# Kernel tuning notes

Measured on AMD Instinct MI355X. Metric: run time of the kernel, lower is better.

The kernel has to match this reference:

```python
import jax, jax.numpy as jnp
import numpy as np

B, T, M, Q = 1024, 336, 1, 9
DFF, H, L = 7, 1024, 2
D_IN = DFF + M      # decoder input per step
D_OUT = M * Q       # quantile outputs per step


def setup_inputs() -> dict:
    key = jax.random.key(0)
    ks = jax.random.split(key, 16)
    s = 1.0 / np.sqrt(H)

    def rn(k, shape, scale):
        return (jax.random.normal(k, shape, jnp.float32) * scale).astype(jnp.float32)

    return {
        "batchsize": B,
        "Y_teacher": rn(ks[0], (B, T, M), 1.0),
        "inp_y": rn(ks[1], (B, 1, M), 1.0),
        "h": rn(ks[2], (L, B, H), 0.1),
        "c": rn(ks[3], (L, B, H), 0.1),
        "future_features": rn(ks[4], (B, T, DFF), 1.0),
        "horizon_span": T,
        "teacher_forcing": 0,
        "teacher_forcing_prob": 0,
        # LSTM layer 0 (input size D_IN) and layer 1 (input size H), PyTorch i,f,g,o gate order
        "W_ih0": rn(ks[5], (4 * H, D_IN), s),
        "W_hh0": rn(ks[6], (4 * H, H), s),
        "b_ih0": rn(ks[7], (4 * H,), s),
        "b_hh0": rn(ks[8], (4 * H,), s),
        "W_ih1": rn(ks[9], (4 * H, H), s),
        "W_hh1": rn(ks[10], (4 * H, H), s),
        "b_ih1": rn(ks[11], (4 * H,), s),
        "b_hh1": rn(ks[12], (4 * H,), s),
        # output projection d_hidden -> M*Q
        "W_out": rn(ks[13], (D_OUT, H), s),
        "b_out": rn(ks[14], (D_OUT,), s),
    }


def reference(batchsize, Y_teacher, inp_y, h, c, future_features, horizon_span,
              teacher_forcing, teacher_forcing_prob,
              W_ih0, W_hh0, b_ih0, b_hh0, W_ih1, W_hh1, b_ih1, b_hh1,
              W_out, b_out):
    m = inp_y.shape[-1]
    Wih = (W_ih0, W_ih1)
    Whh = (W_hh0, W_hh1)
    bih = (b_ih0, b_ih1)
    bhh = (b_hh0, b_hh1)

    def step(carry, f_t):
        hs, cs, y_prev = carry            # hs,cs: [L,B,H]; y_prev: [B,M]; f_t: [B,DFF]
        x = jnp.concatenate([y_prev, f_t], axis=-1)   # [B, D_IN]
        new_h, new_c = [], []
        for l in range(len(Wih)):
            gates = x @ Wih[l].T + bih[l] + hs[l] @ Whh[l].T + bhh[l]  # [B, 4H]
            i_, f_, g_, o_ = jnp.split(gates, 4, axis=-1)
            c_new = jax.nn.sigmoid(f_) * cs[l] + jax.nn.sigmoid(i_) * jnp.tanh(g_)
            h_new = jax.nn.sigmoid(o_) * jnp.tanh(c_new)
            new_h.append(h_new)
            new_c.append(c_new)
            x = h_new
        y = x @ W_out.T + b_out           # [B, M*Q]
        return (jnp.stack(new_h), jnp.stack(new_c), y[:, :m]), y

    ff = jnp.swapaxes(future_features, 0, 1)          # [T, B, DFF]
    _, ys = jax.lax.scan(step, (h, c, inp_y[:, 0, :]), ff)
    out = jnp.swapaxes(ys, 0, 1)                      # [B, T, M*Q]
    return out.reshape(batchsize, horizon_span, m, -1)
```

## Files before the change

kernel.cpp:

```cpp
#include <hip/hip_runtime.h>

typedef _Float16 f16;
typedef __attribute__((ext_vector_type(8))) _Float16 f16x8;
typedef __attribute__((ext_vector_type(4))) float f32x4;

#define NBATCH 1024
#define NH 1024
#define NT 336
#define NDFF 7
#define NQ 9
#define K0 1088
#define K1 2048
#define OUTSTRIDE (NT * NQ)

__device__ __forceinline__ float sigf(float x) { return 1.0f / (1.0f + __expf(-x)); }
__device__ __forceinline__ float tanhfast(float x) { return 1.0f - 2.0f / (__expf(2.0f * x) + 1.0f); }

__device__ __forceinline__ void gll16(const void* g, void* l) {
  __builtin_amdgcn_global_load_lds((const __attribute__((address_space(1))) void*)g,
                                   (__attribute__((address_space(3))) void*)l, 16, 0, 0);
}

__global__ void pack_w0(const float* __restrict__ Wih0, const float* __restrict__ Whh0,
                        f16* __restrict__ Wp0) {
  const int idx = blockIdx.x * 256 + threadIdx.x;
  const int pr = idx / K0;
  const int dk = idx - pr * K0;
  const int cb = pr >> 7, p = pr & 127;
  const int gate = (p >> 4) & 3;
  const int hl = ((p >> 6) << 4) | (p & 15);
  const int j = (gate << 10) + (cb << 5) + hl;
  const int sk = (dk & ~63) | ((dk & 63) ^ ((p & 7) << 3));
  float v;
  if (sk < 8) v = Wih0[j * 8 + sk];
  else if (sk < 64) v = 0.0f;
  else v = Whh0[(size_t)j * NH + (sk - 64)];
  Wp0[idx] = (f16)v;
}

__global__ void pack_w1(const float* __restrict__ Wih1, const float* __restrict__ Whh1,
                        f16* __restrict__ Wp1) {
  const int idx = blockIdx.x * 256 + threadIdx.x;
  const int pr = idx >> 11;
  const int dk = idx & 2047;
  const int cb = pr >> 7, p = pr & 127;
  const int gate = (p >> 4) & 3;
  const int hl = ((p >> 6) << 4) | (p & 15);
  const int j = (gate << 10) + (cb << 5) + hl;
  const int sk = (dk & ~63) | ((dk & 63) ^ ((p & 7) << 3));
  const float v = (sk < 1024) ? Wih1[(size_t)j * NH + sk]
                              : Whh1[(size_t)j * NH + (sk - 1024)];
  Wp1[idx] = (f16)v;
}

__global__ void pack_bias(const float* __restrict__ a0, const float* __restrict__ b0,
                          const float* __restrict__ a1, const float* __restrict__ b1,
                          float* __restrict__ bias0, float* __restrict__ bias1) {
  const int j = blockIdx.x * 256 + threadIdx.x;
  if (j < 4096) { bias0[j] = a0[j] + b0[j]; bias1[j] = a1[j] + b1[j]; }
}

__global__ void init_state(const float* __restrict__ h_in, const float* __restrict__ c_in,
                           f16* __restrict__ h0, f16* __restrict__ h1,
                           float* __restrict__ c0, float* __restrict__ c1) {
  const int idx = blockIdx.x * 256 + threadIdx.x;
  const int l = idx >> 20;
  const int rc = idx & 1048575;
  const int row = rc >> 10;
  const int dk = idx & 1023;
  const int sk = (dk & ~63) | ((dk & 63) ^ ((row & 7) << 3));
  const float hv = h_in[((size_t)l << 20) + ((size_t)row << 10) + sk];
  if (l == 0) { h0[rc] = (f16)hv; c0[rc] = c_in[idx]; }
  else        { h1[rc] = (f16)hv; c1[rc] = c_in[idx]; }
}

__global__ void final_y(const float* __restrict__ ypartT, const float* __restrict__ bout,
                        float* __restrict__ dout) {
  const int idx = blockIdx.x * 256 + threadIdx.x;
  const int row = idx & 1023;
  const int q = idx >> 10;
  float s = bout[q];
#pragma unroll
  for (int nb2 = 0; nb2 < 32; ++nb2) s += ypartT[(((q << 5) + nb2) << 10) + row];
  dout[(size_t)row * OUTSTRIDE + 335 * NQ + q] = s;
}

template <int IS_S1>
__global__ __launch_bounds__(256, 1) void step_kernel(
    const f16* __restrict__ Wp, const float* __restrict__ bias,
    const f16* __restrict__ hA, const f16* __restrict__ hA2,
    float* __restrict__ cbuf, f16* __restrict__ hout,
    const float* __restrict__ ff, const float* __restrict__ inpy,
    float* __restrict__ ypartT, const float* __restrict__ Wout,
    const float* __restrict__ bout, float* __restrict__ dout, int t) {
  constexpr int KDIM = IS_S1 ? K1 : K0;
  constexpr int NKT = KDIM / 64;
  constexpr int LDSZ = IS_S1 ? (98304 + 128 * 33 * 4) : 98304;
  __shared__ __align__(16) unsigned char lds8[LDSZ];

  const int tid = threadIdx.x;
  const int wv = tid >> 6;
  const int ln = tid & 63;
  const int wr = wv >> 1, wc = wv & 1;
  const int blk = blockIdx.x;
  const int rb = (blk >> 3) & 7;
  const int cb = (blk & 7) * 4 + (blk >> 6);
  const int row0 = rb * 128;
  const int hcol0 = cb * 32;

  auto stageB = [&](int kt, int buf) {
#pragma unroll
    for (int i = 0; i < 4; ++i) {
      const int ci = wv * 4 + i;
      const int tr = ci * 8 + (ln >> 3);
      const f16* g = Wp + (size_t)(cb * 128 + tr) * KDIM + kt * 64 + (ln & 7) * 8;
      gll16(g, lds8 + buf * 32768 + 16384 + ci * 1024);
    }
  };
  auto stageA = [&](int kt, int buf) {
    const f16* src;
    int kb;
    if (IS_S1) {
      if (kt < 16) { src = hA; kb = kt * 64; }
      else { src = hA2; kb = (kt - 16) * 64; }
    } else { src = hA; kb = (kt - 1) * 64; }
#pragma unroll
    for (int i = 0; i < 4; ++i) {
      const int ci = wv * 4 + i;
      const int r = ci * 8 + (ln >> 3);
      const f16* g = src + (size_t)(row0 + r) * NH + kb + (ln & 7) * 8;
      gll16(g, lds8 + buf * 32768 + ci * 1024);
    }
  };

  if (!IS_S1) {
    if (tid < 128) {
      const int row = row0 + tid;
      float y0;
      if (t == 0) {
        y0 = inpy[row];
      } else {
        y0 = bout[0];
        const float* yp = ypartT + row;
#pragma unroll
        for (int nb2 = 0; nb2 < 32; ++nb2) y0 += yp[nb2 << 10];
      }
      const float* fsrc = ff + ((size_t)row * NT + t) * NDFF;
      f16x8 xv;
      xv[0] = (f16)y0;
#pragma unroll
      for (int jj = 0; jj < 7; ++jj) xv[1 + jj] = (f16)fsrc[jj];
      *(f16x8*)(lds8 + tid * 128 + ((tid & 7) << 4)) = xv;
    }
    f16x8 zv;
#pragma unroll
    for (int jj = 0; jj < 8; ++jj) zv[jj] = (f16)0.0f;
    for (int idx = tid; idx < 128 * 7; idx += 256) {
      const int r = idx / 7;
      const int ch = 1 + (idx - r * 7);
      *(f16x8*)(lds8 + r * 128 + ((ch ^ (r & 7)) << 4)) = zv;
    }
    if (t > 0 && cb < NQ && tid < 128) {
      const int q = cb;
      const int row = row0 + tid;
      float s = bout[q];
      const float* yp = ypartT + ((size_t)(q << 5) << 10) + row;
#pragma unroll
      for (int nb2 = 0; nb2 < 32; ++nb2) s += yp[nb2 << 10];
      dout[(size_t)row * OUTSTRIDE + (t - 1) * NQ + q] = s;
    }
    stageB(0, 0);
    stageA(1, 1); stageB(1, 1);
  } else {
    stageA(0, 0); stageB(0, 0);
    stageA(1, 1); stageB(1, 1);
  }
  asm volatile("s_waitcnt lgkmcnt(0)" ::: "memory");

  f32x4 acc[4][4];
  const f32x4 zf = {0.0f, 0.0f, 0.0f, 0.0f};
#pragma unroll
  for (int m = 0; m < 4; ++m)
#pragma unroll
    for (int n = 0; n < 4; ++n) acc[m][n] = zf;

  const int lanerow = ln & 15;
  const int xm = (ln & 7) << 4;
  const int kgrp = (ln >> 4) << 4;
  int bc = 0;

  for (int kt = 0; kt < NKT; ++kt) {
    __builtin_amdgcn_sched_barrier(0);
    if (kt + 1 < NKT) {
      asm volatile("s_waitcnt vmcnt(8)" ::: "memory");
    } else {
      asm volatile("s_waitcnt vmcnt(0)" ::: "memory");
    }
    __builtin_amdgcn_s_barrier();
    __builtin_amdgcn_sched_barrier(0);
    if (kt + 2 < NKT) {
      const int nb = (bc == 0) ? 2 : bc - 1;
      stageA(kt + 2, nb);
      stageB(kt + 2, nb);
    }
    const unsigned char* Ab = lds8 + bc * 32768;
    const unsigned char* Bb = Ab + 16384;
#pragma unroll
    for (int ks = 0; ks < 2; ++ks) {
      const int kb = (kgrp + ks * 64) ^ xm;
      f16x8 afr[4], bfr[4];
#pragma unroll
      for (int m = 0; m < 4; ++m)
        afr[m] = *(const f16x8*)(Ab + (wr * 64 + m * 16 + lanerow) * 128 + kb);
#pragma unroll
      for (int n = 0; n < 4; ++n)
        bfr[n] = *(const f16x8*)(Bb + (wc * 64 + n * 16 + lanerow) * 128 + kb);
      __builtin_amdgcn_s_setprio(1);
#pragma unroll
      for (int m = 0; m < 4; ++m)
#pragma unroll
        for (int n = 0; n < 4; ++n)
          acc[m][n] = __builtin_amdgcn_mfma_f32_16x16x32_f16(afr[m], bfr[n], acc[m][n], 0, 0, 0);
      __builtin_amdgcn_s_setprio(0);
    }
    bc = (bc == 2) ? 0 : bc + 1;
  }

  float* hbuf = (float*)(lds8 + 98304);
  const int hcol = hcol0 + wc * 16 + lanerow;
  const float bi = bias[hcol];
  const float bff = bias[NH + hcol];
  const float bg = bias[2 * NH + hcol];
  const float bo = bias[3 * NH + hcol];
#pragma unroll
  for (int m = 0; m < 4; ++m) {
    const f32x4 vi = acc[m][0];
    const f32x4 vf = acc[m][1];
    const f32x4 vg = acc[m][2];
    const f32x4 vo = acc[m][3];
#pragma unroll
    for (int r = 0; r < 4; ++r) {
      const int rloc = wr * 64 + m * 16 + ((ln >> 4) << 2) + r;
      const int row = row0 + rloc;
      const size_t cidx = (size_t)row * NH + hcol;
      const float c_old = cbuf[cidx];
      const float ig = sigf(vi[r] + bi);
      const float fg = sigf(vf[r] + bff);
      const float gg = tanhfast(vg[r] + bg);
      const float og = sigf(vo[r] + bo);
      const float cn = fg * c_old + ig * gg;
      const float hn = og * tanhfast(cn);
      cbuf[cidx] = cn;
      *(f16*)((unsigned char*)hout + (size_t)row * 2048 + ((hcol >> 6) << 7) +
              (((hcol & 63) << 1) ^ ((row & 7) << 4))) = (f16)hn;
      if (IS_S1) hbuf[rloc * 33 + wc * 16 + lanerow] = hn;
    }
  }
  if (IS_S1) {
    __syncthreads();
    for (int task = tid; task < 128 * NQ; task += 256) {
      const int rloc = task & 127;
      const int q = task >> 7;
      const float* wq = Wout + q * NH + hcol0;
      float s = 0.0f;
#pragma unroll
      for (int c2 = 0; c2 < 32; ++c2) s += hbuf[rloc * 33 + c2] * wq[c2];
      ypartT[(size_t)((q << 5) + cb) * 1024 + row0 + rloc] = s;
    }
  }
}

extern "C" void kernel_launch(void* const* d_in, const int* in_sizes, int n_in,
                              void* d_out, int out_size, void* d_ws, size_t ws_size,
                              hipStream_t stream) {
  const float* inpy = (const float*)d_in[2];
  const float* h_in = (const float*)d_in[3];
  const float* c_in = (const float*)d_in[4];
  const float* ff   = (const float*)d_in[5];
  const float* Wih0 = (const float*)d_in[9];
  const float* Whh0 = (const float*)d_in[10];
  const float* bih0 = (const float*)d_in[11];
  const float* bhh0 = (const float*)d_in[12];
  const float* Wih1 = (const float*)d_in[13];
  const float* Whh1 = (const float*)d_in[14];
  const float* bih1 = (const float*)d_in[15];
  const float* bhh1 = (const float*)d_in[16];
  const float* Wout = (const float*)d_in[17];
  const float* bout = (const float*)d_in[18];
  float* dout = (float*)d_out;

  unsigned char* ws = (unsigned char*)d_ws;
  size_t off = 0;
  auto alloc = [&](size_t bytes) -> void* {
    void* p = ws + off;
    off += (bytes + 255) & ~(size_t)255;
    return p;
  };
  f16* Wp0 = (f16*)alloc((size_t)4096 * K0 * 2);
  f16* Wp1 = (f16*)alloc((size_t)4096 * K1 * 2);
  f16* h0b0 = (f16*)alloc((size_t)NBATCH * NH * 2);
  f16* h0b1 = (f16*)alloc((size_t)NBATCH * NH * 2);
  f16* h1b0 = (f16*)alloc((size_t)NBATCH * NH * 2);
  f16* h1b1 = (f16*)alloc((size_t)NBATCH * NH * 2);
  float* c0 = (float*)alloc((size_t)NBATCH * NH * 4);
  float* c1 = (float*)alloc((size_t)NBATCH * NH * 4);
  float* bias0 = (float*)alloc(4096 * 4);
  float* bias1 = (float*)alloc(4096 * 4);
  float* ypartT = (float*)alloc((size_t)NQ * 32 * 1024 * 4);
  f16* h0b[2] = {h0b0, h0b1};
  f16* h1b[2] = {h1b0, h1b1};

  pack_w0<<<(4096 * K0) / 256, 256, 0, stream>>>(Wih0, Whh0, Wp0);
  pack_w1<<<(4096 * K1) / 256, 256, 0, stream>>>(Wih1, Whh1, Wp1);
  pack_bias<<<16, 256, 0, stream>>>(bih0, bhh0, bih1, bhh1, bias0, bias1);
  init_state<<<(2 * NBATCH * NH) / 256, 256, 0, stream>>>(h_in, c_in, h0b[0], h1b[0], c0, c1);

  for (int t = 0; t < NT; ++t) {
    const int p = t & 1;
    step_kernel<0><<<256, 256, 0, stream>>>(Wp0, bias0, h0b[p], nullptr, c0, h0b[1 - p],
                                            ff, inpy, ypartT, nullptr, bout, dout, t);
    step_kernel<1><<<256, 256, 0, stream>>>(Wp1, bias1, h0b[1 - p], h1b[p], c1, h1b[1 - p],
                                            nullptr, nullptr, ypartT, Wout, bout, dout, t);
  }
  final_y<<<36, 256, 0, stream>>>(ypartT, bout, dout);
}
```

Measured before the change: 15.05 ms.

## Replace per-step kernel launches with one persistent kernel using per-row-block counters

Fuses the 672 per-timestep launches into a single persistent kernel of 256 blocks. Blocks synchronise through per-row-block atomic counters with spin-waits, and the cell states stay in registers for all steps. Loads of the next layer's weights and of the h tiles are software-pipelined across layer boundaries, so the global barriers overlap with useful work. In exchange it depends on all 256 blocks being co-resident and on correct cross-block memory visibility (h loads use cache-bypass bits), which risks deadlock or stale reads.

```diff
diff --git a/kernel.cpp b/kernel.cpp
--- a/kernel.cpp
+++ b/kernel.cpp
@@ -16,9 +16,19 @@
 __device__ __forceinline__ float sigf(float x) { return 1.0f / (1.0f + __expf(-x)); }
 __device__ __forceinline__ float tanhfast(float x) { return 1.0f - 2.0f / (__expf(2.0f * x) + 1.0f); }
 
-__device__ __forceinline__ void gll16(const void* g, void* l) {
+__device__ __forceinline__ void gll_w(const void* g, void* l) {
   __builtin_amdgcn_global_load_lds((const __attribute__((address_space(1))) void*)g,
                                    (__attribute__((address_space(3))) void*)l, 16, 0, 0);
+}
+__device__ __forceinline__ void gll_c(const void* g, void* l) {
+  __builtin_amdgcn_global_load_lds((const __attribute__((address_space(1))) void*)g,
+                                   (__attribute__((address_space(3))) void*)l, 16, 0, 17);
+}
+
+__device__ __forceinline__ void spinGE(unsigned int* c, unsigned int tgt) {
+  while (__hip_atomic_load(c, __ATOMIC_RELAXED, __HIP_MEMORY_SCOPE_AGENT) < tgt) {
+    __builtin_amdgcn_s_sleep(2);
+  }
 }
 
 __global__ void pack_w0(const float* __restrict__ Wih0, const float* __restrict__ Whh0,
@@ -53,16 +63,17 @@
   Wp1[idx] = (f16)v;
 }
 
-__global__ void pack_bias(const float* __restrict__ a0, const float* __restrict__ b0,
+__global__ void pack_misc(const float* __restrict__ a0, const float* __restrict__ b0,
                           const float* __restrict__ a1, const float* __restrict__ b1,
-                          float* __restrict__ bias0, float* __restrict__ bias1) {
+                          float* __restrict__ bias0, float* __restrict__ bias1,
+                          unsigned int* __restrict__ cnt) {
   const int j = blockIdx.x * 256 + threadIdx.x;
   if (j < 4096) { bias0[j] = a0[j] + b0[j]; bias1[j] = a1[j] + b1[j]; }
-}
-
-__global__ void init_state(const float* __restrict__ h_in, const float* __restrict__ c_in,
-                           f16* __restrict__ h0, f16* __restrict__ h1,
-                           float* __restrict__ c0, float* __restrict__ c1) {
+  if (j < 16) cnt[j] = 0;
+}
+
+__global__ void init_h(const float* __restrict__ h_in,
+                       f16* __restrict__ h0, f16* __restrict__ h1) {
   const int idx = blockIdx.x * 256 + threadIdx.x;
   const int l = idx >> 20;
   const int rc = idx & 1048575;
@@ -70,8 +81,8 @@
   const int dk = idx & 1023;
   const int sk = (dk & ~63) | ((dk & 63) ^ ((row & 7) << 3));
   const float hv = h_in[((size_t)l << 20) + ((size_t)row << 10) + sk];
-  if (l == 0) { h0[rc] = (f16)hv; c0[rc] = c_in[idx]; }
-  else        { h1[rc] = (f16)hv; c1[rc] = c_in[idx]; }
+  if (l == 0) h0[rc] = (f16)hv;
+  else        h1[rc] = (f16)hv;
 }
 
 __global__ void final_y(const float* __restrict__ ypartT, const float* __restrict__ bout,
@@ -85,18 +96,18 @@
   dout[(size_t)row * OUTSTRIDE + 335 * NQ + q] = s;
 }
 
-template <int IS_S1>
-__global__ __launch_bounds__(256, 1) void step_kernel(
-    const f16* __restrict__ Wp, const float* __restrict__ bias,
-    const f16* __restrict__ hA, const f16* __restrict__ hA2,
-    float* __restrict__ cbuf, f16* __restrict__ hout,
+__global__ __launch_bounds__(256, 1) void persist(
+    const f16* __restrict__ Wp0, const f16* __restrict__ Wp1,
+    const float* __restrict__ bias0, const float* __restrict__ bias1,
+    f16* __restrict__ h0b0, f16* __restrict__ h0b1,
+    f16* __restrict__ h1b0, f16* __restrict__ h1b1,
+    unsigned int* __restrict__ cnt,
     const float* __restrict__ ff, const float* __restrict__ inpy,
     float* __restrict__ ypartT, const float* __restrict__ Wout,
-    const float* __restrict__ bout, float* __restrict__ dout, int t) {
-  constexpr int KDIM = IS_S1 ? K1 : K0;
-  constexpr int NKT = KDIM / 64;
-  constexpr int LDSZ = IS_S1 ? (98304 + 128 * 33 * 4) : 98304;
-  __shared__ __align__(16) unsigned char lds8[LDSZ];
+    const float* __restrict__ bout, const float* __restrict__ c_in,
+    float* __restrict__ dout) {
+  __shared__ __align__(16) unsigned char lds8[98304 + 128 * 33 * 4];
+  float* hbuf = (float*)(lds8 + 98304);
 
   const int tid = threadIdx.x;
   const int wv = tid >> 6;
@@ -107,75 +118,50 @@
   const int cb = (blk & 7) * 4 + (blk >> 6);
   const int row0 = rb * 128;
   const int hcol0 = cb * 32;
-
-  auto stageB = [&](int kt, int buf) {
+  unsigned int* aCnt = cnt + rb;
+  unsigned int* bCnt = cnt + 8 + rb;
+
+  f16* h0arr[2] = {h0b0, h0b1};
+  f16* h1arr[2] = {h1b0, h1b1};
+
+  const int lanerow = ln & 15;
+  const int xm = (ln & 7) << 4;
+  const int kgrp = (ln >> 4) << 4;
+  const int hcol = hcol0 + wc * 16 + lanerow;
+
+  float c0r[4][4], c1r[4][4];
+#pragma unroll
+  for (int m = 0; m < 4; ++m)
+#pragma unroll
+    for (int r = 0; r < 4; ++r) {
+      const int row = row0 + wr * 64 + m * 16 + ((ln >> 4) << 2) + r;
+      c0r[m][r] = c_in[(size_t)row * NH + hcol];
+      c1r[m][r] = c_in[(size_t)(NBATCH * NH) + (size_t)row * NH + hcol];
+    }
+
+  const float b0i = bias0[hcol], b0f = bias0[NH + hcol],
+              b0g = bias0[2 * NH + hcol], b0o = bias0[3 * NH + hcol];
+  const float b1i = bias1[hcol], b1f = bias1[NH + hcol],
+              b1g = bias1[2 * NH + hcol], b1o = bias1[3 * NH + hcol];
+
+  auto stW = [&](const f16* W, int KDIM, int kt, int buf) {
 #pragma unroll
     for (int i = 0; i < 4; ++i) {
       const int ci = wv * 4 + i;
       const int tr = ci * 8 + (ln >> 3);
-      const f16* g = Wp + (size_t)(cb * 128 + tr) * KDIM + kt * 64 + (ln & 7) * 8;
-      gll16(g, lds8 + buf * 32768 + 16384 + ci * 1024);
+      gll_w(W + (size_t)(cb * 128 + tr) * KDIM + kt * 64 + (ln & 7) * 8,
+            lds8 + buf * 32768 + 16384 + ci * 1024);
     }
   };
-  auto stageA = [&](int kt, int buf) {
-    const f16* src;
-    int kb;
-    if (IS_S1) {
-      if (kt < 16) { src = hA; kb = kt * 64; }
-      else { src = hA2; kb = (kt - 16) * 64; }
-    } else { src = hA; kb = (kt - 1) * 64; }
+  auto stH = [&](const f16* h, int kb, int buf) {
 #pragma unroll
     for (int i = 0; i < 4; ++i) {
       const int ci = wv * 4 + i;
       const int r = ci * 8 + (ln >> 3);
-      const f16* g = src + (size_t)(row0 + r) * NH + kb + (ln & 7) * 8;
-      gll16(g, lds8 + buf * 32768 + ci * 1024);
+      gll_c(h + (((size_t)(row0 + r)) << 10) + kb + (ln & 7) * 8,
+            lds8 + buf * 32768 + ci * 1024);
     }
   };
-
-  if (!IS_S1) {
-    if (tid < 128) {
-      const int row = row0 + tid;
-      float y0;
-      if (t == 0) {
-        y0 = inpy[row];
-      } else {
-        y0 = bout[0];
-        const float* yp = ypartT + row;
-#pragma unroll
-        for (int nb2 = 0; nb2 < 32; ++nb2) y0 += yp[nb2 << 10];
-      }
-      const float* fsrc = ff + ((size_t)row * NT + t) * NDFF;
-      f16x8 xv;
-      xv[0] = (f16)y0;
-#pragma unroll
-      for (int jj = 0; jj < 7; ++jj) xv[1 + jj] = (f16)fsrc[jj];
-      *(f16x8*)(lds8 + tid * 128 + ((tid & 7) << 4)) = xv;
-    }
-    f16x8 zv;
-#pragma unroll
-    for (int jj = 0; jj < 8; ++jj) zv[jj] = (f16)0.0f;
-    for (int idx = tid; idx < 128 * 7; idx += 256) {
-      const int r = idx / 7;
-      const int ch = 1 + (idx - r * 7);
-      *(f16x8*)(lds8 + r * 128 + ((ch ^ (r & 7)) << 4)) = zv;
-    }
-    if (t > 0 && cb < NQ && tid < 128) {
-      const int q = cb;
-      const int row = row0 + tid;
-      float s = bout[q];
-      const float* yp = ypartT + ((size_t)(q << 5) << 10) + row;
-#pragma unroll
-      for (int nb2 = 0; nb2 < 32; ++nb2) s += yp[nb2 << 10];
-      dout[(size_t)row * OUTSTRIDE + (t - 1) * NQ + q] = s;
-    }
-    stageB(0, 0);
-    stageA(1, 1); stageB(1, 1);
-  } else {
-    stageA(0, 0); stageB(0, 0);
-    stageA(1, 1); stageB(1, 1);
-  }
-  asm volatile("s_waitcnt lgkmcnt(0)" ::: "memory");
 
   f32x4 acc[4][4];
   const f32x4 zf = {0.0f, 0.0f, 0.0f, 0.0f};
@@ -184,26 +170,8 @@
 #pragma unroll
     for (int n = 0; n < 4; ++n) acc[m][n] = zf;
 
-  const int lanerow = ln & 15;
-  const int xm = (ln & 7) << 4;
-  const int kgrp = (ln >> 4) << 4;
-  int bc = 0;
-
-  for (int kt = 0; kt < NKT; ++kt) {
-    __builtin_amdgcn_sched_barrier(0);
-    if (kt + 1 < NKT) {
-      asm volatile("s_waitcnt vmcnt(8)" ::: "memory");
-    } else {
-      asm volatile("s_waitcnt vmcnt(0)" ::: "memory");
-    }
-    __builtin_amdgcn_s_barrier();
-    __builtin_amdgcn_sched_barrier(0);
-    if (kt + 2 < NKT) {
-      const int nb = (bc == 0) ? 2 : bc - 1;
-      stageA(kt + 2, nb);
-      stageB(kt + 2, nb);
-    }
-    const unsigned char* Ab = lds8 + bc * 32768;
+  auto compute = [&](int bufc) {
+    const unsigned char* Ab = lds8 + bufc * 32768;
     const unsigned char* Bb = Ab + 16384;
 #pragma unroll
     for (int ks = 0; ks < 2; ++ks) {
@@ -223,40 +191,153 @@
           acc[m][n] = __builtin_amdgcn_mfma_f32_16x16x32_f16(afr[m], bfr[n], acc[m][n], 0, 0, 0);
       __builtin_amdgcn_s_setprio(0);
     }
-    bc = (bc == 2) ? 0 : bc + 1;
-  }
-
-  float* hbuf = (float*)(lds8 + 98304);
-  const int hcol = hcol0 + wc * 16 + lanerow;
-  const float bi = bias[hcol];
-  const float bff = bias[NH + hcol];
-  const float bg = bias[2 * NH + hcol];
-  const float bo = bias[3 * NH + hcol];
-#pragma unroll
-  for (int m = 0; m < 4; ++m) {
-    const f32x4 vi = acc[m][0];
-    const f32x4 vf = acc[m][1];
-    const f32x4 vg = acc[m][2];
-    const f32x4 vo = acc[m][3];
-#pragma unroll
-    for (int r = 0; r < 4; ++r) {
-      const int rloc = wr * 64 + m * 16 + ((ln >> 4) << 2) + r;
-      const int row = row0 + rloc;
-      const size_t cidx = (size_t)row * NH + hcol;
-      const float c_old = cbuf[cidx];
-      const float ig = sigf(vi[r] + bi);
-      const float fg = sigf(vf[r] + bff);
-      const float gg = tanhfast(vg[r] + bg);
-      const float og = sigf(vo[r] + bo);
-      const float cn = fg * c_old + ig * gg;
-      const float hn = og * tanhfast(cn);
-      cbuf[cidx] = cn;
-      *(f16*)((unsigned char*)hout + (size_t)row * 2048 + ((hcol >> 6) << 7) +
-              (((hcol & 63) << 1) ^ ((row & 7) << 4))) = (f16)hn;
-      if (IS_S1) hbuf[rloc * 33 + wc * 16 + lanerow] = hn;
-    }
-  }
-  if (IS_S1) {
+  };
+
+  stH(h0arr[0], 0, 0);  stW(Wp0, K0, 1, 0);
+  stH(h0arr[0], 64, 1); stW(Wp0, K0, 2, 1);
+
+  int sb = 0;
+
+  for (int t = 0; t < NT; ++t) {
+    const int p = t & 1;
+    const f16* h0prev = h0arr[p];
+    f16* h0new = h0arr[1 - p];
+    const f16* h1prev = h1arr[p];
+    f16* h1new = h1arr[1 - p];
+
+    for (int it = 0; it < 17; ++it) {
+      __builtin_amdgcn_sched_barrier(0);
+      if (it == 15) asm volatile("s_waitcnt vmcnt(4) lgkmcnt(0)" ::: "memory");
+      else          asm volatile("s_waitcnt vmcnt(8) lgkmcnt(0)" ::: "memory");
+      __builtin_amdgcn_s_barrier();
+      __builtin_amdgcn_sched_barrier(0);
+      const int bufc = sb;
+      const int bufs = (sb + 2 >= 3) ? sb - 1 : sb + 2;
+
+      if (it == 14) {
+        if (t > 0) {
+          if (tid == 0) spinGE(bCnt, 32u * (unsigned)t);
+          __builtin_amdgcn_s_barrier();
+          __builtin_amdgcn_sched_barrier(0);
+        }
+        unsigned char* xb = lds8 + bufs * 32768;
+        if (tid < 128) {
+          const int row = row0 + tid;
+          float y0;
+          if (t == 0) {
+            y0 = inpy[row];
+          } else {
+            y0 = bout[0];
+#pragma unroll
+            for (int nb2 = 0; nb2 < 32; ++nb2)
+              y0 += __hip_atomic_load(ypartT + (nb2 << 10) + row,
+                                      __ATOMIC_RELAXED, __HIP_MEMORY_SCOPE_AGENT);
+          }
+          const float* fsrc = ff + ((size_t)row * NT + t) * NDFF;
+          f16x8 xv;
+          xv[0] = (f16)y0;
+#pragma unroll
+          for (int jj = 0; jj < 7; ++jj) xv[1 + jj] = (f16)fsrc[jj];
+          *(f16x8*)(xb + tid * 128 + ((tid & 7) << 4)) = xv;
+        }
+        f16x8 zv;
+#pragma unroll
+        for (int jj = 0; jj < 8; ++jj) zv[jj] = (f16)0.0f;
+        for (int idx = tid; idx < 128 * 7; idx += 256) {
+          const int r = idx / 7;
+          const int ch = 1 + (idx - r * 7);
+          *(f16x8*)(xb + r * 128 + ((ch ^ (r & 7)) << 4)) = zv;
+        }
+        if (t > 0 && cb < NQ && tid < 128) {
+          const int row = row0 + tid;
+          float s = bout[cb];
+#pragma unroll
+          for (int nb2 = 0; nb2 < 32; ++nb2)
+            s += __hip_atomic_load(ypartT + (((cb << 5) + nb2) << 10) + row,
+                                   __ATOMIC_RELAXED, __HIP_MEMORY_SCOPE_AGENT);
+          dout[(size_t)row * OUTSTRIDE + (t - 1) * NQ + cb] = s;
+        }
+        stW(Wp0, K0, 0, bufs);
+      } else {
+        const int s = it + 2;
+        if (s <= 15)      { stH(h0prev, s * 64, bufs); stW(Wp0, K0, s + 1, bufs); }
+        else if (s == 17) { stH(h1prev, 0, bufs);      stW(Wp1, K1, 16, bufs); }
+        else              { stH(h1prev, 64, bufs);     stW(Wp1, K1, 17, bufs); }
+      }
+      compute(bufc);
+      sb = (bufc + 1 >= 3) ? 0 : bufc + 1;
+    }
+
+#pragma unroll
+    for (int m = 0; m < 4; ++m) {
+      const f32x4 vi = acc[m][0], vf = acc[m][1], vg = acc[m][2], vo = acc[m][3];
+#pragma unroll
+      for (int r = 0; r < 4; ++r) {
+        const int rloc = wr * 64 + m * 16 + ((ln >> 4) << 2) + r;
+        const int row = row0 + rloc;
+        const float ig = sigf(vi[r] + b0i);
+        const float fg = sigf(vf[r] + b0f);
+        const float gg = tanhfast(vg[r] + b0g);
+        const float og = sigf(vo[r] + b0o);
+        const float cn = fg * c0r[m][r] + ig * gg;
+        c0r[m][r] = cn;
+        const f16 hn = (f16)(og * tanhfast(cn));
+        unsigned short hb = __builtin_bit_cast(unsigned short, hn);
+        unsigned short* dst = (unsigned short*)((unsigned char*)h0new + (size_t)row * 2048 +
+                              ((hcol >> 6) << 7) + (((hcol & 63) << 1) ^ ((row & 7) << 4)));
+        __hip_atomic_store(dst, hb, __ATOMIC_RELAXED, __HIP_MEMORY_SCOPE_AGENT);
+      }
+      acc[m][0] = zf; acc[m][1] = zf; acc[m][2] = zf; acc[m][3] = zf;
+    }
+    asm volatile("s_waitcnt vmcnt(0)" ::: "memory");
+    __syncthreads();
+    if (tid == 0)
+      __hip_atomic_fetch_add(aCnt, 1u, __ATOMIC_RELAXED, __HIP_MEMORY_SCOPE_AGENT);
+
+    for (int it = 0; it < 32; ++it) {
+      __builtin_amdgcn_sched_barrier(0);
+      asm volatile("s_waitcnt vmcnt(8) lgkmcnt(0)" ::: "memory");
+      __builtin_amdgcn_s_barrier();
+      __builtin_amdgcn_sched_barrier(0);
+      const int bufc = sb;
+      const int bufs = (sb + 2 >= 3) ? sb - 1 : sb + 2;
+
+      if (it == 14) {
+        if (tid == 0) spinGE(aCnt, 32u * (unsigned)(t + 1));
+        __builtin_amdgcn_s_barrier();
+        __builtin_amdgcn_sched_barrier(0);
+      }
+      const int s = it + 2;
+      if (s <= 15)      { stH(h1prev, s * 64, bufs);       stW(Wp1, K1, 16 + s, bufs); }
+      else if (s <= 31) { stH(h0new, (s - 16) * 64, bufs); stW(Wp1, K1, s - 16, bufs); }
+      else              { stH(h0new, (s - 32) * 64, bufs); stW(Wp0, K0, s - 31, bufs); }
+      compute(bufc);
+      sb = (bufc + 1 >= 3) ? 0 : bufc + 1;
+    }
+
+#pragma unroll
+    for (int m = 0; m < 4; ++m) {
+      const f32x4 vi = acc[m][0], vf = acc[m][1], vg = acc[m][2], vo = acc[m][3];
+#pragma unroll
+      for (int r = 0; r < 4; ++r) {
+        const int rloc = wr * 64 + m * 16 + ((ln >> 4) << 2) + r;
+        const int row = row0 + rloc;
+        const float ig = sigf(vi[r] + b1i);
+        const float fg = sigf(vf[r] + b1f);
+        const float gg = tanhfast(vg[r] + b1g);
+        const float og = sigf(vo[r] + b1o);
+        const float cn = fg * c1r[m][r] + ig * gg;
+        c1r[m][r] = cn;
+        const float hnf = og * tanhfast(cn);
+        const f16 hn = (f16)hnf;
+        unsigned short hb = __builtin_bit_cast(unsigned short, hn);
+        unsigned short* dst = (unsigned short*)((unsigned char*)h1new + (size_t)row * 2048 +
+                              ((hcol >> 6) << 7) + (((hcol & 63) << 1) ^ ((row & 7) << 4)));
+        __hip_atomic_store(dst, hb, __ATOMIC_RELAXED, __HIP_MEMORY_SCOPE_AGENT);
+        hbuf[rloc * 33 + wc * 16 + lanerow] = hnf;
+      }
+      acc[m][0] = zf; acc[m][1] = zf; acc[m][2] = zf; acc[m][3] = zf;
+    }
     __syncthreads();
     for (int task = tid; task < 128 * NQ; task += 256) {
       const int rloc = task & 127;
@@ -265,8 +346,13 @@
       float s = 0.0f;
 #pragma unroll
       for (int c2 = 0; c2 < 32; ++c2) s += hbuf[rloc * 33 + c2] * wq[c2];
-      ypartT[(size_t)((q << 5) + cb) * 1024 + row0 + rloc] = s;
-    }
+      __hip_atomic_store(ypartT + (size_t)((q << 5) + cb) * 1024 + row0 + rloc, s,
+                         __ATOMIC_RELAXED, __HIP_MEMORY_SCOPE_AGENT);
+    }
+    asm volatile("s_waitcnt vmcnt(0)" ::: "memory");
+    __syncthreads();
+    if (tid == 0)
+      __hip_atomic_fetch_add(bCnt, 1u, __ATOMIC_RELAXED, __HIP_MEMORY_SCOPE_AGENT);
   }
 }
 
@@ -302,25 +388,18 @@
   f16* h0b1 = (f16*)alloc((size_t)NBATCH * NH * 2);
   f16* h1b0 = (f16*)alloc((size_t)NBATCH * NH * 2);
   f16* h1b1 = (f16*)alloc((size_t)NBATCH * NH * 2);
-  float* c0 = (float*)alloc((size_t)NBATCH * NH * 4);
-  float* c1 = (float*)alloc((size_t)NBATCH * NH * 4);
   float* bias0 = (float*)alloc(4096 * 4);
   float* bias1 = (float*)alloc(4096 * 4);
   float* ypartT = (float*)alloc((size_t)NQ * 32 * 1024 * 4);
-  f16* h0b[2] = {h0b0, h0b1};
-  f16* h1b[2] = {h1b0, h1b1};
+  unsigned int* cnt = (unsigned int*)alloc(64);
 
   pack_w0<<<(4096 * K0) / 256, 256, 0, stream>>>(Wih0, Whh0, Wp0);
   pack_w1<<<(4096 * K1) / 256, 256, 0, stream>>>(Wih1, Whh1, Wp1);
-  pack_bias<<<16, 256, 0, stream>>>(bih0, bhh0, bih1, bhh1, bias0, bias1);
-  init_state<<<(2 * NBATCH * NH) / 256, 256, 0, stream>>>(h_in, c_in, h0b[0], h1b[0], c0, c1);
-
-  for (int t = 0; t < NT; ++t) {
-    const int p = t & 1;
-    step_kernel<0><<<256, 256, 0, stream>>>(Wp0, bias0, h0b[p], nullptr, c0, h0b[1 - p],
-                                            ff, inpy, ypartT, nullptr, bout, dout, t);
-    step_kernel<1><<<256, 256, 0, stream>>>(Wp1, bias1, h0b[1 - p], h1b[p], c1, h1b[1 - p],
-                                            nullptr, nullptr, ypartT, Wout, bout, dout, t);
-  }
+  pack_misc<<<16, 256, 0, stream>>>(bih0, bhh0, bih1, bhh1, bias0, bias1, cnt);
+  init_h<<<(2 * NBATCH * NH) / 256, 256, 0, stream>>>(h_in, h0b0, h1b0);
+
+  persist<<<256, 256, 0, stream>>>(Wp0, Wp1, bias0, bias1, h0b0, h0b1, h1b0, h1b1,
+                                   cnt, ff, inpy, ypartT, Wout, bout, c_in, dout);
+
   final_y<<<36, 256, 0, stream>>>(ypartT, bout, dout);
 }
```

Result: slower. 18.93 ms (+25.7%).

## Use 128-wide K tiles, lane-packed cell state and LDS-staged vector h stores

Applied to the files above, without the earlier changes.

Each K stage now covers 128 elements and uses two buffers instead of three 64-wide buffers, waiting for all loads and barriering once per stage. Layer 0's 8-wide input chunk gets its own LDS area and is computed first. The fp32 cell state is repacked at init so each lane reads and writes contiguous addresses, replacing scattered row-major accesses. New h values are staged through LDS and written as 16-byte f16 vectors instead of single scattered f16 stores. The aim is fewer barriers and more coalesced state traffic, but a full vmcnt(0) wait every stage may hide less load latency.

```diff
diff --git a/kernel.cpp b/kernel.cpp
--- a/kernel.cpp
+++ b/kernel.cpp
@@ -12,11 +12,12 @@
 #define K0 1088
 #define K1 2048
 #define OUTSTRIDE (NT * NQ)
+#define XAOFF 131072
 
 __device__ __forceinline__ float sigf(float x) { return 1.0f / (1.0f + __expf(-x)); }
 __device__ __forceinline__ float tanhfast(float x) { return 1.0f - 2.0f / (__expf(2.0f * x) + 1.0f); }
 
-__device__ __forceinline__ void gll16(const void* g, void* l) {
+__device__ __forceinline__ void gll(const void* g, void* l) {
   __builtin_amdgcn_global_load_lds((const __attribute__((address_space(1))) void*)g,
                                    (__attribute__((address_space(3))) void*)l, 16, 0, 0);
 }
@@ -60,9 +61,8 @@
   if (j < 4096) { bias0[j] = a0[j] + b0[j]; bias1[j] = a1[j] + b1[j]; }
 }
 
-__global__ void init_state(const float* __restrict__ h_in, const float* __restrict__ c_in,
-                           f16* __restrict__ h0, f16* __restrict__ h1,
-                           float* __restrict__ c0, float* __restrict__ c1) {
+__global__ void init_h(const float* __restrict__ h_in,
+                       f16* __restrict__ h0, f16* __restrict__ h1) {
   const int idx = blockIdx.x * 256 + threadIdx.x;
   const int l = idx >> 20;
   const int rc = idx & 1048575;
@@ -70,8 +70,24 @@
   const int dk = idx & 1023;
   const int sk = (dk & ~63) | ((dk & 63) ^ ((row & 7) << 3));
   const float hv = h_in[((size_t)l << 20) + ((size_t)row << 10) + sk];
-  if (l == 0) { h0[rc] = (f16)hv; c0[rc] = c_in[idx]; }
-  else        { h1[rc] = (f16)hv; c1[rc] = c_in[idx]; }
+  if (l == 0) h0[rc] = (f16)hv;
+  else        h1[rc] = (f16)hv;
+}
+
+__global__ void init_c(const float* __restrict__ c_in, float* __restrict__ c0p,
+                       float* __restrict__ c1p) {
+  const int idx = blockIdx.x * 256 + threadIdx.x;
+  const int l = idx >> 20;
+  const int rem = idx & 1048575;
+  const int ln = rem & 63;
+  const int j = (rem >> 6) & 15;
+  const int wv = (rem >> 10) & 3;
+  const int cb = (rem >> 12) & 31;
+  const int rb = rem >> 17;
+  const int row = rb * 128 + (wv >> 1) * 64 + (j >> 2) * 16 + ((ln >> 4) & 3) * 4 + (j & 3);
+  const int col = cb * 32 + (wv & 1) * 16 + (ln & 15);
+  const float v = c_in[((size_t)l << 20) + ((size_t)row << 10) + col];
+  if (l == 0) c0p[rem] = v; else c1p[rem] = v;
 }
 
 __global__ void final_y(const float* __restrict__ ypartT, const float* __restrict__ bout,
@@ -85,18 +101,17 @@
   dout[(size_t)row * OUTSTRIDE + 335 * NQ + q] = s;
 }
 
-template <int IS_S1>
+template <int L>
 __global__ __launch_bounds__(256, 1) void step_kernel(
     const f16* __restrict__ Wp, const float* __restrict__ bias,
-    const f16* __restrict__ hA, const f16* __restrict__ hA2,
-    float* __restrict__ cbuf, f16* __restrict__ hout,
+    const f16* __restrict__ hA0, const f16* __restrict__ hA1,
+    f16* __restrict__ hout, float* __restrict__ cpk,
     const float* __restrict__ ff, const float* __restrict__ inpy,
     float* __restrict__ ypartT, const float* __restrict__ Wout,
     const float* __restrict__ bout, float* __restrict__ dout, int t) {
-  constexpr int KDIM = IS_S1 ? K1 : K0;
-  constexpr int NKT = KDIM / 64;
-  constexpr int LDSZ = IS_S1 ? (98304 + 128 * 33 * 4) : 98304;
-  __shared__ __align__(16) unsigned char lds8[LDSZ];
+  constexpr int KDIM = L ? K1 : K0;
+  constexpr int NTILE = L ? 16 : 9;
+  __shared__ __align__(16) unsigned char lds8[147456];
 
   const int tid = threadIdx.x;
   const int wv = tid >> 6;
@@ -108,32 +123,66 @@
   const int row0 = rb * 128;
   const int hcol0 = cb * 32;
 
-  auto stageB = [&](int kt, int buf) {
-#pragma unroll
-    for (int i = 0; i < 4; ++i) {
-      const int ci = wv * 4 + i;
-      const int tr = ci * 8 + (ln >> 3);
-      const f16* g = Wp + (size_t)(cb * 128 + tr) * KDIM + kt * 64 + (ln & 7) * 8;
-      gll16(g, lds8 + buf * 32768 + 16384 + ci * 1024);
+  const int lanerow = ln & 15;
+  const int xm = (ln & 7) << 4;
+  const int kgrp = (ln >> 4) << 4;
+  const int hcol = hcol0 + wc * 16 + lanerow;
+
+  auto stage128 = [&](int j, int slot) {
+    const f16* hsrc; int koff, wk0;
+    if (L) {
+      if (j < 8) { hsrc = hA0; koff = j * 128; } else { hsrc = hA1; koff = (j - 8) * 128; }
+      wk0 = j * 128;
+    } else {
+      hsrc = hA0; koff = (j - 1) * 128; wk0 = 64 + (j - 1) * 128;
+    }
+    unsigned char* sb = lds8 + slot * 65536;
+#pragma unroll
+    for (int ii = 0; ii < 8; ++ii) {
+      const int ci = wv * 8 + ii;
+      const int r = ci * 4 + (ln >> 4);
+      gll(hsrc + (((size_t)(row0 + r)) << 10) + koff + (ln & 15) * 8, sb + ci * 1024);
+    }
+#pragma unroll
+    for (int ii = 0; ii < 8; ++ii) {
+      const int ci = wv * 8 + ii;
+      const int pr = ci * 4 + (ln >> 4);
+      gll(Wp + (size_t)(cb * 128 + pr) * KDIM + wk0 + (ln & 15) * 8,
+          sb + 32768 + ci * 1024);
     }
   };
-  auto stageA = [&](int kt, int buf) {
-    const f16* src;
-    int kb;
-    if (IS_S1) {
-      if (kt < 16) { src = hA; kb = kt * 64; }
-      else { src = hA2; kb = (kt - 16) * 64; }
-    } else { src = hA; kb = (kt - 1) * 64; }
-#pragma unroll
-    for (int i = 0; i < 4; ++i) {
-      const int ci = wv * 4 + i;
-      const int r = ci * 8 + (ln >> 3);
-      const f16* g = src + (size_t)(row0 + r) * NH + kb + (ln & 7) * 8;
-      gll16(g, lds8 + buf * 32768 + ci * 1024);
+
+  f32x4 acc[4][4];
+  const f32x4 zf = {0.0f, 0.0f, 0.0f, 0.0f};
+#pragma unroll
+  for (int m = 0; m < 4; ++m)
+#pragma unroll
+    for (int n = 0; n < 4; ++n) acc[m][n] = zf;
+
+  auto compute128 = [&](int slot) {
+    const unsigned char* Ab = lds8 + slot * 65536;
+    const unsigned char* Bb = Ab + 32768;
+#pragma unroll
+    for (int ks = 0; ks < 4; ++ks) {
+      const int kb = ((ks >> 1) << 7) + ((kgrp + ((ks & 1) << 6)) ^ xm);
+      f16x8 afr[4], bfr[4];
+#pragma unroll
+      for (int m = 0; m < 4; ++m)
+        afr[m] = *(const f16x8*)(Ab + (wr * 64 + m * 16 + lanerow) * 256 + kb);
+#pragma unroll
+      for (int n = 0; n < 4; ++n)
+        bfr[n] = *(const f16x8*)(Bb + (wc * 64 + n * 16 + lanerow) * 256 + kb);
+      __builtin_amdgcn_s_setprio(1);
+#pragma unroll
+      for (int m = 0; m < 4; ++m)
+#pragma unroll
+        for (int n = 0; n < 4; ++n)
+          acc[m][n] = __builtin_amdgcn_mfma_f32_16x16x32_f16(afr[m], bfr[n], acc[m][n], 0, 0, 0);
+      __builtin_amdgcn_s_setprio(0);
     }
   };
 
-  if (!IS_S1) {
+  if (!L) {
     if (tid < 128) {
       const int row = row0 + tid;
       float y0;
@@ -150,7 +199,7 @@
       xv[0] = (f16)y0;
 #pragma unroll
       for (int jj = 0; jj < 7; ++jj) xv[1 + jj] = (f16)fsrc[jj];
-      *(f16x8*)(lds8 + tid * 128 + ((tid & 7) << 4)) = xv;
+      *(f16x8*)(lds8 + XAOFF + tid * 128 + ((tid & 7) << 4)) = xv;
     }
     f16x8 zv;
 #pragma unroll
@@ -158,113 +207,111 @@
     for (int idx = tid; idx < 128 * 7; idx += 256) {
       const int r = idx / 7;
       const int ch = 1 + (idx - r * 7);
-      *(f16x8*)(lds8 + r * 128 + ((ch ^ (r & 7)) << 4)) = zv;
+      *(f16x8*)(lds8 + XAOFF + r * 128 + ((ch ^ (r & 7)) << 4)) = zv;
     }
     if (t > 0 && cb < NQ && tid < 128) {
-      const int q = cb;
       const int row = row0 + tid;
-      float s = bout[q];
-      const float* yp = ypartT + ((size_t)(q << 5) << 10) + row;
+      float s = bout[cb];
+      const float* yp = ypartT + ((size_t)(cb << 5) << 10) + row;
 #pragma unroll
       for (int nb2 = 0; nb2 < 32; ++nb2) s += yp[nb2 << 10];
-      dout[(size_t)row * OUTSTRIDE + (t - 1) * NQ + q] = s;
-    }
-    stageB(0, 0);
-    stageA(1, 1); stageB(1, 1);
+      dout[(size_t)row * OUTSTRIDE + (t - 1) * NQ + cb] = s;
+    }
+#pragma unroll
+    for (int ii = 0; ii < 4; ++ii) {
+      const int ci = wv * 4 + ii;
+      gll(Wp + (size_t)(cb * 128 + ci * 8 + (ln >> 3)) * KDIM + (ln & 7) * 8,
+          lds8 + 32768 + ci * 1024);
+    }
   } else {
-    stageA(0, 0); stageB(0, 0);
-    stageA(1, 1); stageB(1, 1);
-  }
-  asm volatile("s_waitcnt lgkmcnt(0)" ::: "memory");
-
-  f32x4 acc[4][4];
-  const f32x4 zf = {0.0f, 0.0f, 0.0f, 0.0f};
-#pragma unroll
-  for (int m = 0; m < 4; ++m)
-#pragma unroll
-    for (int n = 0; n < 4; ++n) acc[m][n] = zf;
-
-  const int lanerow = ln & 15;
-  const int xm = (ln & 7) << 4;
-  const int kgrp = (ln >> 4) << 4;
-  int bc = 0;
-
-  for (int kt = 0; kt < NKT; ++kt) {
+    stage128(0, 0);
+  }
+  asm volatile("s_waitcnt vmcnt(0) lgkmcnt(0)" ::: "memory");
+  __builtin_amdgcn_s_barrier();
+
+#pragma unroll 1
+  for (int i = 0; i < NTILE; ++i) {
     __builtin_amdgcn_sched_barrier(0);
-    if (kt + 1 < NKT) {
-      asm volatile("s_waitcnt vmcnt(8)" ::: "memory");
+    if (i + 1 < NTILE) stage128(i + 1, (i + 1) & 1);
+    __builtin_amdgcn_sched_barrier(0);
+    if (!L && i == 0) {
+      const unsigned char* Ab = lds8 + XAOFF;
+      const unsigned char* Bb = lds8 + 32768;
+#pragma unroll
+      for (int ks = 0; ks < 2; ++ks) {
+        const int kb = (kgrp + (ks << 6)) ^ xm;
+        f16x8 afr[4], bfr[4];
+#pragma unroll
+        for (int m = 0; m < 4; ++m)
+          afr[m] = *(const f16x8*)(Ab + (wr * 64 + m * 16 + lanerow) * 128 + kb);
+#pragma unroll
+        for (int n = 0; n < 4; ++n)
+          bfr[n] = *(const f16x8*)(Bb + (wc * 64 + n * 16 + lanerow) * 128 + kb);
+        __builtin_amdgcn_s_setprio(1);
+#pragma unroll
+        for (int m = 0; m < 4; ++m)
+#pragma unroll
+          for (int n = 0; n < 4; ++n)
+            acc[m][n] = __builtin_amdgcn_mfma_f32_16x16x32_f16(afr[m], bfr[n], acc[m][n], 0, 0, 0);
+        __builtin_amdgcn_s_setprio(0);
+      }
     } else {
-      asm volatile("s_waitcnt vmcnt(0)" ::: "memory");
-    }
+      compute128(i & 1);
+    }
+    __builtin_amdgcn_sched_barrier(0);
+    asm volatile("s_waitcnt vmcnt(0)" ::: "memory");
     __builtin_amdgcn_s_barrier();
     __builtin_amdgcn_sched_barrier(0);
-    if (kt + 2 < NKT) {
-      const int nb = (bc == 0) ? 2 : bc - 1;
-      stageA(kt + 2, nb);
-      stageB(kt + 2, nb);
-    }
-    const unsigned char* Ab = lds8 + bc * 32768;
-    const unsigned char* Bb = Ab + 16384;
-#pragma unroll
-    for (int ks = 0; ks < 2; ++ks) {
-      const int kb = (kgrp + ks * 64) ^ xm;
-      f16x8 afr[4], bfr[4];
-#pragma unroll
-      for (int m = 0; m < 4; ++m)
-        afr[m] = *(const f16x8*)(Ab + (wr * 64 + m * 16 + lanerow) * 128 + kb);
-#pragma unroll
-      for (int n = 0; n < 4; ++n)
-        bfr[n] = *(const f16x8*)(Bb + (wc * 64 + n * 16 + lanerow) * 128 + kb);
-      __builtin_amdgcn_s_setprio(1);
-#pragma unroll
-      for (int m = 0; m < 4; ++m)
-#pragma unroll
-        for (int n = 0; n < 4; ++n)
-          acc[m][n] = __builtin_amdgcn_mfma_f32_16x16x32_f16(afr[m], bfr[n], acc[m][n], 0, 0, 0);
-      __builtin_amdgcn_s_setprio(0);
-    }
-    bc = (bc == 2) ? 0 : bc + 1;
-  }
-
-  float* hbuf = (float*)(lds8 + 98304);
-  const int hcol = hcol0 + wc * 16 + lanerow;
+  }
+
+  float* hb = (float*)(lds8 + (L ? 0 : 65536));
   const float bi = bias[hcol];
-  const float bff = bias[NH + hcol];
+  const float bf = bias[NH + hcol];
   const float bg = bias[2 * NH + hcol];
   const float bo = bias[3 * NH + hcol];
+  const int cbase = ((rb * 32 + cb) * 4 + wv) * 1024;
 #pragma unroll
   for (int m = 0; m < 4; ++m) {
-    const f32x4 vi = acc[m][0];
-    const f32x4 vf = acc[m][1];
-    const f32x4 vg = acc[m][2];
-    const f32x4 vo = acc[m][3];
+    const f32x4 vi = acc[m][0], vf = acc[m][1], vg = acc[m][2], vo = acc[m][3];
 #pragma unroll
     for (int r = 0; r < 4; ++r) {
+      const int j = m * 4 + r;
       const int rloc = wr * 64 + m * 16 + ((ln >> 4) << 2) + r;
-      const int row = row0 + rloc;
-      const size_t cidx = (size_t)row * NH + hcol;
-      const float c_old = cbuf[cidx];
+      const float c_old = cpk[cbase + j * 64 + ln];
       const float ig = sigf(vi[r] + bi);
-      const float fg = sigf(vf[r] + bff);
+      const float fg = sigf(vf[r] + bf);
       const float gg = tanhfast(vg[r] + bg);
       const float og = sigf(vo[r] + bo);
       const float cn = fg * c_old + ig * gg;
-      const float hn = og * tanhfast(cn);
-      cbuf[cidx] = cn;
-      *(f16*)((unsigned char*)hout + (size_t)row * 2048 + ((hcol >> 6) << 7) +
-              (((hcol & 63) << 1) ^ ((row & 7) << 4))) = (f16)hn;
-      if (IS_S1) hbuf[rloc * 33 + wc * 16 + lanerow] = hn;
-    }
-  }
-  if (IS_S1) {
-    __syncthreads();
+      cpk[cbase + j * 64 + ln] = cn;
+      hb[rloc * 36 + wc * 16 + lanerow] = og * tanhfast(cn);
+    }
+  }
+  asm volatile("s_waitcnt lgkmcnt(0)" ::: "memory");
+  __builtin_amdgcn_s_barrier();
+#pragma unroll
+  for (int u2 = 0; u2 < 2; ++u2) {
+    const int unit = tid * 2 + u2;
+    const int r = unit >> 2;
+    const int u = unit & 3;
+    const f32x4 lo = *(const f32x4*)(hb + r * 36 + u * 8);
+    const f32x4 hi = *(const f32x4*)(hb + r * 36 + u * 8 + 4);
+    f16x8 v;
+#pragma unroll
+    for (int jj = 0; jj < 4; ++jj) { v[jj] = (f16)lo[jj]; v[4 + jj] = (f16)hi[jj]; }
+    const int rowg = row0 + r;
+    const int pb = ((hcol0 & 63) << 1) + u * 16;
+    *(f16x8*)((unsigned char*)hout + (size_t)rowg * 2048 + ((hcol0 >> 6) << 7) +
+              (pb ^ ((rowg & 7) << 4))) = v;
+  }
+  if (L) {
     for (int task = tid; task < 128 * NQ; task += 256) {
       const int rloc = task & 127;
       const int q = task >> 7;
       const float* wq = Wout + q * NH + hcol0;
       float s = 0.0f;
 #pragma unroll
-      for (int c2 = 0; c2 < 32; ++c2) s += hbuf[rloc * 33 + c2] * wq[c2];
+      for (int c2 = 0; c2 < 32; ++c2) s += hb[rloc * 36 + c2] * wq[c2];
       ypartT[(size_t)((q << 5) + cb) * 1024 + row0 + rloc] = s;
     }
   }
@@ -302,25 +349,26 @@
   f16* h0b1 = (f16*)alloc((size_t)NBATCH * NH * 2);
   f16* h1b0 = (f16*)alloc((size_t)NBATCH * NH * 2);
   f16* h1b1 = (f16*)alloc((size_t)NBATCH * NH * 2);
-  float* c0 = (float*)alloc((size_t)NBATCH * NH * 4);
-  float* c1 = (float*)alloc((size_t)NBATCH * NH * 4);
   float* bias0 = (float*)alloc(4096 * 4);
   float* bias1 = (float*)alloc(4096 * 4);
   float* ypartT = (float*)alloc((size_t)NQ * 32 * 1024 * 4);
+  float* c0p = (float*)alloc((size_t)NBATCH * NH * 4);
+  float* c1p = (float*)alloc((size_t)NBATCH * NH * 4);
   f16* h0b[2] = {h0b0, h0b1};
   f16* h1b[2] = {h1b0, h1b1};
 
   pack_w0<<<(4096 * K0) / 256, 256, 0, stream>>>(Wih0, Whh0, Wp0);
   pack_w1<<<(4096 * K1) / 256, 256, 0, stream>>>(Wih1, Whh1, Wp1);
   pack_bias<<<16, 256, 0, stream>>>(bih0, bhh0, bih1, bhh1, bias0, bias1);
-  init_state<<<(2 * NBATCH * NH) / 256, 256, 0, stream>>>(h_in, c_in, h0b[0], h1b[0], c0, c1);
+  init_h<<<(2 * NBATCH * NH) / 256, 256, 0, stream>>>(h_in, h0b0, h1b0);
+  init_c<<<(2 * NBATCH * NH) / 256, 256, 0, stream>>>(c_in, c0p, c1p);
 
   for (int t = 0; t < NT; ++t) {
     const int p = t & 1;
-    step_kernel<0><<<256, 256, 0, stream>>>(Wp0, bias0, h0b[p], nullptr, c0, h0b[1 - p],
-                                            ff, inpy, ypartT, nullptr, bout, dout, t);
-    step_kernel<1><<<256, 256, 0, stream>>>(Wp1, bias1, h0b[1 - p], h1b[p], c1, h1b[1 - p],
-                                            nullptr, nullptr, ypartT, Wout, bout, dout, t);
+    step_kernel<0><<<256, 256, 0, stream>>>(Wp0, bias0, h0b[p], nullptr, h0b[1 - p],
+                                            c0p, ff, inpy, ypartT, nullptr, bout, dout, t);
+    step_kernel<1><<<256, 256, 0, stream>>>(Wp1, bias1, h0b[1 - p], h1b[p], h1b[1 - p],
+                                            c1p, nullptr, nullptr, ypartT, Wout, bout, dout, t);
   }
   final_y<<<36, 256, 0, stream>>>(ypartT, bout, dout);
 }
```

Measured after the change: 16.39 ms. 1.09x slower.
